# Kernel optimization log

Hardware: AMD Instinct MI355X
Metric: run time of the kernel (lower is better)

## Reference

```python
import jax, jax.numpy as jnp
import numpy as np

N_NODES = 50000
N_EDGES = 800000
D_FEAT = 128
HIDDEN = 128
BERT_DIM = 768
BATCH = 4096
MAX_ENT = 20
COMB = BERT_DIM + HIDDEN  # 896


def setup_inputs() -> dict:
    key = jax.random.key(0)
    ks = jax.random.split(key, 12)
    article_bert_embeddings = jax.random.normal(ks[0], (BATCH, BERT_DIM), dtype=jnp.float32)
    x = jax.random.normal(ks[1], (N_NODES, D_FEAT), dtype=jnp.float32)
    edge_index = jax.random.randint(ks[2], (2, N_EDGES), 0, N_NODES, dtype=jnp.int64)
    entity_map = jax.random.randint(ks[3], (BATCH, MAX_ENT), 0, N_NODES, dtype=jnp.int64)
    pad = jax.random.uniform(ks[4], (BATCH, MAX_ENT)) < 0.3
    entity_map = jnp.where(pad, jnp.int64(-1), entity_map)
    s = 1.0 / np.sqrt(D_FEAT)
    W1 = jax.random.normal(ks[5], (D_FEAT, HIDDEN), dtype=jnp.float32) * s
    b1 = jnp.zeros((HIDDEN,), dtype=jnp.float32)
    W2 = jax.random.normal(ks[6], (HIDDEN, HIDDEN), dtype=jnp.float32) * (1.0 / np.sqrt(HIDDEN))
    b2 = jnp.zeros((HIDDEN,), dtype=jnp.float32)
    fc1_w = jax.random.normal(ks[7], (COMB, COMB // 2), dtype=jnp.float32) * (1.0 / np.sqrt(COMB))
    fc1_b = jnp.zeros((COMB // 2,), dtype=jnp.float32)
    fc2_w = jax.random.normal(ks[8], (COMB // 2, 1), dtype=jnp.float32) * (1.0 / np.sqrt(COMB // 2))
    fc2_b = jnp.zeros((1,), dtype=jnp.float32)
    return dict(article_bert_embeddings=article_bert_embeddings, x=x,
                edge_index=edge_index, entity_map=entity_map,
                W1=W1, b1=b1, W2=W2, b2=b2,
                fc1_w=fc1_w, fc1_b=fc1_b, fc2_w=fc2_w, fc2_b=fc2_b)


def _gcn_norm(edge_index, n_nodes):
    # add self loops (PyG GCNConv default) and compute symmetric normalization
    loops = jnp.arange(n_nodes, dtype=edge_index.dtype)
    src = jnp.concatenate([edge_index[0], loops])
    dst = jnp.concatenate([edge_index[1], loops])
    deg = jax.ops.segment_sum(jnp.ones_like(dst, dtype=jnp.float32), dst, num_segments=n_nodes)
    dinv = jnp.where(deg > 0, jax.lax.rsqrt(deg), 0.0)
    norm = dinv[src] * dinv[dst]  # [E+N]
    return src, dst, norm


def _gcn_conv(h, W, b, src, dst, norm, n_nodes):
    h = h @ W                                   # [N, H] transform first (cheaper)
    msg = h[src] * norm[:, None]                # [E+N, H] gather
    out = jax.ops.segment_sum(msg, dst, num_segments=n_nodes)
    return out + b


def reference(article_bert_embeddings, x, edge_index, entity_map,
              W1, b1, W2, b2, fc1_w, fc1_b, fc2_w, fc2_b):
    n = x.shape[0]
    src, dst, norm = _gcn_norm(edge_index, n)
    # GNN (dropout in eval mode = identity)
    h = jax.nn.relu(_gcn_conv(x, W1, b1, src, dst, norm, n))
    h = jax.nn.relu(_gcn_conv(h, W2, b2, src, dst, norm, n))
    # ragged mean over entity lists (-1 = padding), fully vectorized
    mask = entity_map >= 0                           # [B, M]
    safe_ids = jnp.where(mask, entity_map, 0)
    gathered = h[safe_ids] * mask[..., None]         # [B, M, H]
    cnt = jnp.maximum(mask.sum(axis=1, keepdims=True).astype(h.dtype), 1.0)
    batch_gnn = gathered.sum(axis=1) / cnt           # [B, H]; rows w/ no entities stay 0
    combined = jnp.concatenate([article_bert_embeddings, batch_gnn], axis=1)
    z = jax.nn.relu(combined @ fc1_w + fc1_b)
    logits = z @ fc2_w + fc2_b
    return jax.nn.sigmoid(logits)
```

## Files before the change

### kernel.cpp

```cpp
#include <hip/hip_runtime.h>
#include <math.h>

typedef __bf16 bf16_t;
typedef __bf16 bfrag8 __attribute__((ext_vector_type(8)));
typedef float  facc4  __attribute__((ext_vector_type(4)));
typedef float  f32x2  __attribute__((ext_vector_type(2)));

#define NBUCK 512
#define BCAP  4096

__device__ inline unsigned short f2b(float x) {
    unsigned int u = __float_as_uint(x);
    unsigned int r = (u + 0x7fffu + ((u >> 16) & 1u)) >> 16;
    return (unsigned short)r;
}
__device__ inline unsigned int pack2(float lo, float hi) {
    return (unsigned int)f2b(lo) | ((unsigned int)f2b(hi) << 16);
}
__device__ inline float blo(unsigned int q) { return __uint_as_float(q << 16); }
__device__ inline float bhi(unsigned int q) { return __uint_as_float(q & 0xffff0000u); }

#if __has_builtin(__builtin_amdgcn_cvt_pk_f32_fp8) && __has_builtin(__builtin_amdgcn_cvt_pk_fp8_f32)
#define HW_FP8 1
#endif

__device__ inline f32x2 fp8pair_dec(unsigned short v) {
#ifdef HW_FP8
    return __builtin_amdgcn_cvt_pk_f32_fp8((int)(unsigned int)v, false);
#else
    f32x2 r;
    unsigned char b0 = (unsigned char)(v & 0xff), b1 = (unsigned char)(v >> 8);
    {
        int e = (b0 >> 3) & 0xf, m = b0 & 7;
        float mag = e ? ldexpf(8.f + m, e - 10) : ldexpf((float)m, -9);
        r.x = (b0 & 0x80) ? -mag : mag;
    }
    {
        int e = (b1 >> 3) & 0xf, m = b1 & 7;
        float mag = e ? ldexpf(8.f + m, e - 10) : ldexpf((float)m, -9);
        r.y = (b1 & 0x80) ? -mag : mag;
    }
    return r;
#endif
}
__device__ inline unsigned char fp8_enc(float x) {
#ifdef HW_FP8
    return (unsigned char)(__builtin_amdgcn_cvt_pk_fp8_f32(x, x, 0, false) & 0xff);
#else
    unsigned char s = (x < 0.f) ? 0x80 : 0;
    float ax = fabsf(x);
    if (!(ax > 0.f)) return s;
    if (ax >= 448.f) return s | 0x7e;
    if (ax < 0.015625f) {
        int q = (int)rintf(ax * 512.f);
        return s | (unsigned char)q;
    }
    int e; float m = frexpf(ax, &e);
    int q = (int)rintf(m * 16.f);
    int E = e - 1;
    if (q == 16) { q = 8; ++E; }
    if (E > 8) return s | 0x7e;
    return s | (unsigned char)(((E + 7) << 3) | (q - 8));
#endif
}

__device__ inline int bucket_of(int d, int N) {
    return (int)(((long long)d * NBUCK) / N);
}

__global__ __launch_bounds__(256) void k_prepbin(const int* __restrict__ src,
                                                 const int* __restrict__ dst,
                                                 int* __restrict__ bcnt,
                                                 unsigned int* __restrict__ ebuf,
                                                 int E, int N,
                                                 const float* __restrict__ bert,
                                                 unsigned int* __restrict__ bertb, int n8,
                                                 const float* __restrict__ W1,
                                                 unsigned short* __restrict__ w1t,
                                                 const float* __restrict__ W2,
                                                 unsigned short* __restrict__ w2t,
                                                 const float* __restrict__ Wf,
                                                 unsigned short* __restrict__ fwt) {
    __shared__ __align__(16) unsigned char smem[23552];
    int bb = blockIdx.x, tid = threadIdx.x;
    int nbin = (E + 4095) / 4096;
    if (bb < nbin) {
        unsigned int* sorted = (unsigned int*)smem;
        int* hist   = (int*)(smem + 16384);
        int* lstart = (int*)(smem + 18432);
        int* gbase  = (int*)(smem + 20480);
        int* sm     = (int*)(smem + 22528);
        int base = bb * 4096;
        int cnt = min(4096, E - base);
        hist[tid] = 0; hist[tid + 256] = 0;
        __syncthreads();
        unsigned int mye[16]; int myb[16];
#pragma unroll
        for (int i = 0; i < 16; ++i) {
            int idx = i * 256 + tid;
            myb[i] = -1;
            if (idx < cnt) {
                int e = base + idx;
                int s = src[e], d = dst[e];
                mye[i] = ((unsigned int)s << 16) | (unsigned int)d;
                int b = bucket_of(d, N);
                myb[i] = b;
                atomicAdd(&hist[b], 1);
            }
        }
        __syncthreads();
        int p0 = hist[2 * tid], p1 = hist[2 * tid + 1];
        sm[tid] = p0 + p1;
        __syncthreads();
        for (int off = 1; off < 256; off <<= 1) {
            int x = (tid >= off) ? sm[tid - off] : 0;
            __syncthreads();
            sm[tid] += x;
            __syncthreads();
        }
        int excl = sm[tid] - (p0 + p1);
        lstart[2 * tid] = excl;
        lstart[2 * tid + 1] = excl + p0;
        __syncthreads();
        hist[tid] = lstart[tid]; hist[tid + 256] = lstart[tid + 256];
        __syncthreads();
#pragma unroll
        for (int i = 0; i < 16; ++i) {
            if (myb[i] >= 0) {
                int pos = atomicAdd(&hist[myb[i]], 1);
                sorted[pos] = mye[i];
            }
        }
        __syncthreads();
        for (int b = tid; b < NBUCK; b += 256) {
            int c = hist[b] - lstart[b];
            gbase[b] = (c > 0) ? atomicAdd(&bcnt[b], c) : 0;
        }
        __syncthreads();
        for (int idx = tid; idx < cnt; idx += 256) {
            unsigned int v = sorted[idx];
            int b = bucket_of((int)(v & 0xffffu), N);
            ebuf[(size_t)b * BCAP + gbase[b] + (idx - lstart[b])] = v;
        }
        return;
    }
    bb -= nbin;
    int ncvt = (n8 + 255) / 256;
    if (bb < ncvt) {
        int i = bb * 256 + tid;
        if (i >= n8) return;
        const float4* p = (const float4*)bert + (size_t)i * 2;
        float4 a = p[0], b = p[1];
        uint4 o;
        o.x = pack2(a.x, a.y);
        o.y = pack2(a.z, a.w);
        o.z = pack2(b.x, b.y);
        o.w = pack2(b.z, b.w);
        ((uint4*)bertb)[i] = o;
        return;
    }
    bb -= ncvt;
    if (bb < 128) {
        int i = bb * 256 + tid;
        const float* W = (i < 16384) ? W1 : W2;
        unsigned short* Wt = (i < 16384) ? w1t : w2t;
        int idx = i & 16383;
        int n = idx >> 7, k = idx & 127;
        Wt[idx] = f2b(W[k * 128 + n]);
        return;
    }
    bb -= 128;
    {
        float* tile = (float*)smem;
        int n0 = (bb % 7) * 64, k0 = (bb / 7) * 64;
#pragma unroll
        for (int i = 0; i < 16; ++i) {
            int idx = i * 256 + tid;
            int r = idx >> 6, c = idx & 63;
            tile[r * 65 + c] = Wf[(size_t)(k0 + r) * 448 + n0 + c];
        }
        __syncthreads();
#pragma unroll
        for (int i = 0; i < 16; ++i) {
            int idx = i * 256 + tid;
            int c = idx >> 6, r = idx & 63;
            fwt[(size_t)(n0 + c) * 896 + k0 + r] = f2b(tile[r * 65 + c]);
        }
    }
}

__global__ __launch_bounds__(256) void k_build2(const unsigned int* __restrict__ ebuf,
                                                const int* __restrict__ bcnt,
                                                int* __restrict__ offs,
                                                float* __restrict__ dinv,
                                                unsigned short* __restrict__ csr,
                                                int N, int E) {
    __shared__ unsigned short seg[BCAP];
    __shared__ int cnt_l[128];
    __shared__ int scan_l[128];
    __shared__ int curs[128];
    __shared__ int smr[256];
    int b = blockIdx.x, tid = threadIdx.x;
    int part = 0;
    for (int j = tid; j < b; j += 256) part += bcnt[j];
    smr[tid] = part;
    __syncthreads();
    for (int off = 128; off > 0; off >>= 1) {
        if (tid < off) smr[tid] += smr[tid + off];
        __syncthreads();
    }
    int base = smr[0];
    int lo = (int)(((long long)b * N + NBUCK - 1) / NBUCK);
    int cnt = bcnt[b];
    int nrange = (int)(((long long)(b + 1) * N + NBUCK - 1) / NBUCK) - lo;
    if (b == 0 && tid == 0) offs[N] = E;
    if (tid < 128) cnt_l[tid] = 0;
    __syncthreads();
    for (int i = tid; i < cnt; i += 256) {
        unsigned int v = ebuf[(size_t)b * BCAP + i];
        atomicAdd(&cnt_l[(int)(v & 0xffffu) - lo], 1);
    }
    __syncthreads();
    if (tid < 128) scan_l[tid] = cnt_l[tid];
    __syncthreads();
    for (int off = 1; off < 128; off <<= 1) {
        int x = 0;
        if (tid < 128 && tid >= off) x = scan_l[tid - off];
        __syncthreads();
        if (tid < 128) scan_l[tid] += x;
        __syncthreads();
    }
    if (tid < 128) {
        int excl = scan_l[tid] - cnt_l[tid];
        curs[tid] = excl;
        if (tid < nrange) {
            offs[lo + tid] = base + excl;
            dinv[lo + tid] = rsqrtf((float)(cnt_l[tid] + 1));
        }
    }
    __syncthreads();
    for (int i = tid; i < cnt; i += 256) {
        unsigned int v = ebuf[(size_t)b * BCAP + i];
        int d = (int)(v & 0xffffu) - lo;
        int p = atomicAdd(&curs[d], 1);
        seg[p] = (unsigned short)(v >> 16);
    }
    __syncthreads();
    for (int i = tid; i < cnt; i += 256) csr[base + i] = seg[i];
}

__global__ __launch_bounds__(256) void k_gemm_f32a(const float* __restrict__ A,
                                                   const bf16_t* __restrict__ Bt,
                                                   const float* __restrict__ rs,
                                                   unsigned char* __restrict__ out8, int M) {
    __shared__ bf16_t As[64 * 136];
    __shared__ bf16_t Bs[128 * 136];
    int t = threadIdx.x;
    int wave = t >> 6, lane = t & 63, quad = lane >> 4, l16 = lane & 15;
    int r0 = blockIdx.x * 64;
#pragma unroll
    for (int i = 0; i < 4; ++i) {
        int chunk = t + i * 256;
        int row = chunk >> 4, c8 = (chunk & 15) << 3;
        int gr = r0 + row;
        float4 a0 = make_float4(0.f, 0.f, 0.f, 0.f), a1 = a0;
        if (gr < M) {
            a0 = *(const float4*)&A[(size_t)gr * 128 + c8];
            a1 = *(const float4*)&A[(size_t)gr * 128 + c8 + 4];
        }
        *(uint4*)&As[row * 136 + c8] =
            make_uint4(pack2(a0.x, a0.y), pack2(a0.z, a0.w),
                       pack2(a1.x, a1.y), pack2(a1.z, a1.w));
    }
#pragma unroll
    for (int i = 0; i < 8; ++i) {
        int chunk = t + i * 256;
        int row = chunk >> 4, c8 = (chunk & 15) << 3;
        *(uint4*)&Bs[row * 136 + c8] = *(const uint4*)&Bt[row * 128 + c8];
    }
    __syncthreads();

    facc4 acc[8];
#pragma unroll
    for (int nt = 0; nt < 8; ++nt) acc[nt] = (facc4){0.f, 0.f, 0.f, 0.f};
    int arow = (wave << 4) + l16;
#pragma unroll
    for (int ks = 0; ks < 4; ++ks) {
        int kk = ks * 32 + quad * 8;
        bfrag8 af = *(const bfrag8*)&As[arow * 136 + kk];
#pragma unroll
        for (int nt = 0; nt < 8; ++nt) {
            bfrag8 bf = *(const bfrag8*)&Bs[(nt * 16 + l16) * 136 + kk];
            acc[nt] = __builtin_amdgcn_mfma_f32_16x16x32_bf16(af, bf, acc[nt], 0, 0, 0);
        }
    }
    __syncthreads();
    unsigned char* f8t = (unsigned char*)As;
    int wrow0 = (wave << 4) + quad * 4;
#pragma unroll
    for (int r = 0; r < 4; ++r) {
        int row = wrow0 + r;
        float sc = rs[min(r0 + row, M - 1)];
#pragma unroll
        for (int nt = 0; nt < 8; ++nt)
            f8t[row * 128 + nt * 16 + l16] = fp8_enc(acc[nt][r] * sc);
    }
    __syncthreads();
#pragma unroll
    for (int i = 0; i < 2; ++i) {
        int idx = t + i * 256;
        int row = idx >> 3, cc = (idx & 7) << 4;
        int gr = r0 + row;
        if (gr < M) *(uint4*)&out8[(size_t)gr * 128 + cc] = *(const uint4*)&f8t[row * 128 + cc];
    }
}

__global__ __launch_bounds__(256) void k_gemm_nn128(const bf16_t* __restrict__ A,
                                                    const bf16_t* __restrict__ Bt,
                                                    const float* __restrict__ rs,
                                                    unsigned char* __restrict__ out8, int M) {
    __shared__ bf16_t As[64 * 136];
    __shared__ bf16_t Bs[128 * 136];
    int t = threadIdx.x;
    int wave = t >> 6, lane = t & 63, quad = lane >> 4, l16 = lane & 15;
    int r0 = blockIdx.x * 64;
#pragma unroll
    for (int i = 0; i < 4; ++i) {
        int chunk = t + i * 256;
        int row = chunk >> 4, c8 = (chunk & 15) << 3;
        int gr = r0 + row;
        uint4 v = make_uint4(0u, 0u, 0u, 0u);
        if (gr < M) v = *(const uint4*)&A[(size_t)gr * 128 + c8];
        *(uint4*)&As[row * 136 + c8] = v;
    }
#pragma unroll
    for (int i = 0; i < 8; ++i) {
        int chunk = t + i * 256;
        int row = chunk >> 4, c8 = (chunk & 15) << 3;
        *(uint4*)&Bs[row * 136 + c8] = *(const uint4*)&Bt[row * 128 + c8];
    }
    __syncthreads();

    facc4 acc[8];
#pragma unroll
    for (int nt = 0; nt < 8; ++nt) acc[nt] = (facc4){0.f, 0.f, 0.f, 0.f};
    int arow = (wave << 4) + l16;
#pragma unroll
    for (int ks = 0; ks < 4; ++ks) {
        int kk = ks * 32 + quad * 8;
        bfrag8 af = *(const bfrag8*)&As[arow * 136 + kk];
#pragma unroll
        for (int nt = 0; nt < 8; ++nt) {
            bfrag8 bf = *(const bfrag8*)&Bs[(nt * 16 + l16) * 136 + kk];
            acc[nt] = __builtin_amdgcn_mfma_f32_16x16x32_bf16(af, bf, acc[nt], 0, 0, 0);
        }
    }
    __syncthreads();
    unsigned char* f8t = (unsigned char*)As;
    int wrow0 = (wave << 4) + quad * 4;
#pragma unroll
    for (int r = 0; r < 4; ++r) {
        int row = wrow0 + r;
        float sc = rs[min(r0 + row, M - 1)];
#pragma unroll
        for (int nt = 0; nt < 8; ++nt)
            f8t[row * 128 + nt * 16 + l16] = fp8_enc(acc[nt][r] * sc);
    }
    __syncthreads();
#pragma unroll
    for (int i = 0; i < 2; ++i) {
        int idx = t + i * 256;
        int row = idx >> 3, cc = (idx & 7) << 4;
        int gr = r0 + row;
        if (gr < M) *(uint4*)&out8[(size_t)gr * 128 + cc] = *(const uint4*)&f8t[row * 128 + cc];
    }
}

__global__ __launch_bounds__(256) void k_agg_b(const unsigned short* __restrict__ hx8,
                                               const unsigned short* __restrict__ csr,
                                               const int* __restrict__ offs,
                                               const float* __restrict__ dinv,
                                               const float* __restrict__ bias,
                                               unsigned int* __restrict__ out, int N) {
    int node = blockIdx.x * 4 + (threadIdx.x >> 6);
    int lane = threadIdx.x & 63;
    if (node >= N) return;
    float di = dinv[node];
    f32x2 sf = fp8pair_dec(hx8[(size_t)node * 64 + lane]);
    float acc0 = sf.x, acc1 = sf.y;
    int s0 = offs[node], s1 = offs[node + 1];
    for (int base = s0; base < s1; base += 64) {
        int nloc = min(64, s1 - base);
        int en = 0;
        if (lane < nloc) en = (int)csr[base + lane];
        int j = 0;
        for (; j + 16 <= nloc; j += 16) {
            int sid[16]; unsigned short g[16];
#pragma unroll
            for (int u = 0; u < 16; ++u) sid[u] = __shfl(en, j + u, 64);
#pragma unroll
            for (int u = 0; u < 16; ++u) g[u] = hx8[(size_t)sid[u] * 64 + lane];
#pragma unroll
            for (int u = 0; u < 16; ++u) { f32x2 d = fp8pair_dec(g[u]); acc0 += d.x; acc1 += d.y; }
        }
        for (; j + 4 <= nloc; j += 4) {
            int sid[4]; unsigned short g[4];
#pragma unroll
            for (int u = 0; u < 4; ++u) sid[u] = __shfl(en, j + u, 64);
#pragma unroll
            for (int u = 0; u < 4; ++u) g[u] = hx8[(size_t)sid[u] * 64 + lane];
#pragma unroll
            for (int u = 0; u < 4; ++u) { f32x2 d = fp8pair_dec(g[u]); acc0 += d.x; acc1 += d.y; }
        }
        for (; j < nloc; ++j) {
            int srcn = __shfl(en, j, 64);
            f32x2 d = fp8pair_dec(hx8[(size_t)srcn * 64 + lane]);
            acc0 += d.x; acc1 += d.y;
        }
    }
    float2 bb = *(const float2*)&bias[lane * 2];
    float v0 = fmaxf(acc0 * di + bb.x, 0.f);
    float v1 = fmaxf(acc1 * di + bb.y, 0.f);
    out[(size_t)node * 64 + lane] = pack2(v0, v1);
}

__global__ __launch_bounds__(256) void k_pool_b(const unsigned int* __restrict__ h,
                                                const int* __restrict__ ent,
                                                unsigned int* __restrict__ out) {
    int r = blockIdx.x * 4 + (threadIdx.x >> 6);
    int lane = threadIdx.x & 63;
    float a0 = 0.f, a1 = 0.f;
    int cnt = 0;
#pragma unroll
    for (int m = 0; m < 20; ++m) {
        int id = ent[r * 20 + m];
        if (id >= 0) {
            unsigned int q = h[(size_t)id * 64 + lane];
            a0 += blo(q); a1 += bhi(q); cnt++;
        }
    }
    float inv = 1.f / (float)max(cnt, 1);
    out[(size_t)r * 64 + lane] = pack2(a0 * inv, a1 * inv);
}

__global__ __launch_bounds__(256) void k_mlp1_mfma(const bf16_t* __restrict__ bertb,
                                                   const bf16_t* __restrict__ gnnb,
                                                   const bf16_t* __restrict__ fwt,
                                                   const float* __restrict__ fb,
                                                   const float* __restrict__ w2,
                                                   float* __restrict__ logacc,
                                                   int* __restrict__ donecnt,
                                                   const float* __restrict__ b2,
                                                   float* __restrict__ outp, int B) {
    __shared__ bf16_t As[64 * 136];
    __shared__ bf16_t Bs[64 * 136];
    __shared__ int lastflag;
    int t = threadIdx.x;
    int wave = t >> 6, lane = t & 63, quad = lane >> 4, l16 = lane & 15;
    int r0 = blockIdx.x * 64, c0 = blockIdx.y * 64;
    facc4 acc[4];
#pragma unroll
    for (int nt = 0; nt < 4; ++nt) acc[nt] = (facc4){0.f, 0.f, 0.f, 0.f};

    for (int ks = 0; ks < 7; ++ks) {
#pragma unroll
        for (int i = 0; i < 4; ++i) {
            int chunk = t + i * 256;
            int row = chunk >> 4, c8 = (chunk & 15) << 3;
            int gr = r0 + row;
            const bf16_t* srcp = (ks < 6) ? &bertb[(size_t)gr * 768 + ks * 128 + c8]
                                          : &gnnb[(size_t)gr * 128 + c8];
            *(uint4*)&As[row * 136 + c8] = *(const uint4*)srcp;
        }
#pragma unroll
        for (int i = 0; i < 4; ++i) {
            int chunk = t + i * 256;
            int row = chunk >> 4, c8 = (chunk & 15) << 3;
            *(uint4*)&Bs[row * 136 + c8] =
                *(const uint4*)&fwt[(size_t)(c0 + row) * 896 + ks * 128 + c8];
        }
        __syncthreads();
        int arow = (wave << 4) + l16;
#pragma unroll
        for (int sub = 0; sub < 4; ++sub) {
            int kk = sub * 32 + quad * 8;
            bfrag8 af = *(const bfrag8*)&As[arow * 136 + kk];
#pragma unroll
            for (int nt = 0; nt < 4; ++nt) {
                bfrag8 bf = *(const bfrag8*)&Bs[(nt * 16 + l16) * 136 + kk];
                acc[nt] = __builtin_amdgcn_mfma_f32_16x16x32_bf16(af, bf, acc[nt], 0, 0, 0);
            }
        }
        __syncthreads();
    }
    int rbase = r0 + (wave << 4) + quad * 4;
    float part[4] = {0.f, 0.f, 0.f, 0.f};
#pragma unroll
    for (int nt = 0; nt < 4; ++nt) {
        int col = c0 + nt * 16 + l16;
        float bb = fb[col];
        float ww = w2[col];
#pragma unroll
        for (int r = 0; r < 4; ++r)
            part[r] += fmaxf(acc[nt][r] + bb, 0.f) * ww;
    }
#pragma unroll
    for (int m = 8; m >= 1; m >>= 1) {
#pragma unroll
        for (int r = 0; r < 4; ++r) part[r] += __shfl_xor(part[r], m, 64);
    }
    if (l16 == 0) {
#pragma unroll
        for (int r = 0; r < 4; ++r) atomicAdd(&logacc[rbase + r], part[r]);
    }
    __threadfence();
    __syncthreads();
    if (t == 0) {
        int done = atomicAdd(donecnt, 1);
        lastflag = (done == (int)(gridDim.x * gridDim.y) - 1);
    }
    __syncthreads();
    if (lastflag) {
        __threadfence();
        float bias2 = b2[0];
        for (int i = t; i < B; i += 256) {
            float v = atomicAdd(&logacc[i], 0.0f);
            outp[i] = 1.f / (1.f + expf(-(v + bias2)));
        }
    }
}

extern "C" void kernel_launch(void* const* d_in, const int* in_sizes, int n_in,
                              void* d_out, int out_size, void* d_ws, size_t ws_size,
                              hipStream_t stream) {
    const float* bert = (const float*)d_in[0];
    const float* x    = (const float*)d_in[1];
    const int*   ei   = (const int*)d_in[2];
    const int*   ent  = (const int*)d_in[3];
    const float* W1   = (const float*)d_in[4];
    const float* b1   = (const float*)d_in[5];
    const float* W2   = (const float*)d_in[6];
    const float* b2   = (const float*)d_in[7];
    const float* fc1w = (const float*)d_in[8];
    const float* fc1b = (const float*)d_in[9];
    const float* fc2w = (const float*)d_in[10];
    const float* fc2b = (const float*)d_in[11];
    float* out = (float*)d_out;

    const int N = in_sizes[1] / 128;
    const int E = in_sizes[2] / 2;
    const int B = in_sizes[0] / 768;

    const int* srcv = ei;
    const int* dstv = ei + E;

    char* wsp = (char*)d_ws;
    size_t off = 0;
    auto alloc = [&](size_t bytes) -> void* {
        void* p = wsp + off;
        off += (bytes + 255) & ~(size_t)255;
        return p;
    };
    int*   bcnt   = (int*)alloc(NBUCK * 4);
    float* logacc = (float*)alloc((size_t)B * 4);
    int*   donecnt= (int*)alloc(4);
    float* dinv   = (float*)alloc((size_t)N * 4);
    int*   offs   = (int*)alloc((size_t)(N + 1) * 4);
    unsigned int*   ebuf  = (unsigned int*)alloc((size_t)NBUCK * BCAP * 4);
    unsigned short* csr16 = (unsigned short*)alloc((size_t)E * 2);
    bf16_t* bertb = (bf16_t*)alloc((size_t)B * 768 * 2);
    bf16_t* w1t   = (bf16_t*)alloc(128 * 128 * 2);
    bf16_t* w2t   = (bf16_t*)alloc(128 * 128 * 2);
    bf16_t* fwt   = (bf16_t*)alloc((size_t)896 * 448 * 2);
    unsigned char* g8buf = (unsigned char*)alloc((size_t)N * 128);
    bf16_t* hbuf  = (bf16_t*)alloc((size_t)N * 128 * 2);
    bf16_t* gnnb  = (bf16_t*)alloc((size_t)B * 128 * 2);
    (void)ws_size; (void)n_in; (void)out_size;

    hipMemsetAsync(bcnt, 0, 2048 + 16384 + 256, stream);

    int nb8 = B * 768 / 8;
    int nbin = (E + 4095) / 4096;
    int nprep = nbin + (nb8 + 255) / 256 + 128 + 98;
    k_prepbin<<<nprep, 256, 0, stream>>>(srcv, dstv, bcnt, ebuf, E, N,
                                         bert, (unsigned int*)bertb, nb8,
                                         W1, (unsigned short*)w1t, W2, (unsigned short*)w2t,
                                         fc1w, (unsigned short*)fwt);
    k_build2<<<NBUCK, 256, 0, stream>>>(ebuf, bcnt, offs, dinv, csr16, N, E);

    int gb = (N + 63) / 64;
    k_gemm_f32a<<<gb, 256, 0, stream>>>(x, w1t, dinv, g8buf, N);
    k_agg_b<<<(N + 3) / 4, 256, 0, stream>>>((const unsigned short*)g8buf, csr16, offs, dinv, b1,
                                             (unsigned int*)hbuf, N);
    k_gemm_nn128<<<gb, 256, 0, stream>>>(hbuf, w2t, dinv, g8buf, N);
    k_agg_b<<<(N + 3) / 4, 256, 0, stream>>>((const unsigned short*)g8buf, csr16, offs, dinv, b2,
                                             (unsigned int*)hbuf, N);
    k_pool_b<<<B / 4, 256, 0, stream>>>((const unsigned int*)hbuf, ent, (unsigned int*)gnnb);
    k_mlp1_mfma<<<dim3(B / 64, 7), 256, 0, stream>>>(bertb, gnnb, fwt, fc1b, fc2w,
                                                     logacc, donecnt, fc2b, out, B);
}
```

Baseline: 243.8 us.

## Prefetch next K-slice into registers and halve MLP row tile in fc1 kernel

The fc1 MFMA kernel now uses 32-row tiles with 128 threads, which doubles the grid from 64x7 to 128x7 blocks so more CUs are busy. It also software-pipelines the K loop: the global loads for the next 128-wide K slice go into registers while MFMAs run on the current slice in LDS. The aim is to hide global-memory latency and improve occupancy. In exchange each block reloads the weight tile (B) for only half as many rows, and register use rises from the prefetch buffers.

```diff
diff --git a/kernel.cpp b/kernel.cpp
--- a/kernel.cpp
+++ b/kernel.cpp
@@ -443,7 +443,7 @@
     out[(size_t)r * 64 + lane] = pack2(a0 * inv, a1 * inv);
 }
 
-__global__ __launch_bounds__(256) void k_mlp1_mfma(const bf16_t* __restrict__ bertb,
+__global__ __launch_bounds__(128) void k_mlp1_mfma(const bf16_t* __restrict__ bertb,
                                                    const bf16_t* __restrict__ gnnb,
                                                    const bf16_t* __restrict__ fwt,
                                                    const float* __restrict__ fb,
@@ -452,34 +452,53 @@
                                                    int* __restrict__ donecnt,
                                                    const float* __restrict__ b2,
                                                    float* __restrict__ outp, int B) {
-    __shared__ bf16_t As[64 * 136];
+    __shared__ bf16_t As[32 * 136];
     __shared__ bf16_t Bs[64 * 136];
     __shared__ int lastflag;
     int t = threadIdx.x;
     int wave = t >> 6, lane = t & 63, quad = lane >> 4, l16 = lane & 15;
-    int r0 = blockIdx.x * 64, c0 = blockIdx.y * 64;
+    int r0 = blockIdx.x * 32, c0 = blockIdx.y * 64;
     facc4 acc[4];
 #pragma unroll
     for (int nt = 0; nt < 4; ++nt) acc[nt] = (facc4){0.f, 0.f, 0.f, 0.f};
 
+    uint4 pa[4], pb[8];
+#define LOAD_A(ks) do { \
+    _Pragma("unroll") \
+    for (int i = 0; i < 4; ++i) { \
+        int chunk = t + i * 128; \
+        int row = chunk >> 4, c8 = (chunk & 15) << 3; \
+        int gr = r0 + row; \
+        const bf16_t* srcp = ((ks) < 6) ? &bertb[(size_t)gr * 768 + (ks) * 128 + c8] \
+                                        : &gnnb[(size_t)gr * 128 + c8]; \
+        pa[i] = *(const uint4*)srcp; \
+    } } while (0)
+#define LOAD_B(ks) do { \
+    _Pragma("unroll") \
+    for (int i = 0; i < 8; ++i) { \
+        int chunk = t + i * 128; \
+        int row = chunk >> 4, c8 = (chunk & 15) << 3; \
+        pb[i] = *(const uint4*)&fwt[(size_t)(c0 + row) * 896 + (ks) * 128 + c8]; \
+    } } while (0)
+#define STORE_AB() do { \
+    _Pragma("unroll") \
+    for (int i = 0; i < 4; ++i) { \
+        int chunk = t + i * 128; \
+        int row = chunk >> 4, c8 = (chunk & 15) << 3; \
+        *(uint4*)&As[row * 136 + c8] = pa[i]; \
+    } \
+    _Pragma("unroll") \
+    for (int i = 0; i < 8; ++i) { \
+        int chunk = t + i * 128; \
+        int row = chunk >> 4, c8 = (chunk & 15) << 3; \
+        *(uint4*)&Bs[row * 136 + c8] = pb[i]; \
+    } } while (0)
+
+    LOAD_A(0); LOAD_B(0);
+    STORE_AB();
+    __syncthreads();
     for (int ks = 0; ks < 7; ++ks) {
-#pragma unroll
-        for (int i = 0; i < 4; ++i) {
-            int chunk = t + i * 256;
-            int row = chunk >> 4, c8 = (chunk & 15) << 3;
-            int gr = r0 + row;
-            const bf16_t* srcp = (ks < 6) ? &bertb[(size_t)gr * 768 + ks * 128 + c8]
-                                          : &gnnb[(size_t)gr * 128 + c8];
-            *(uint4*)&As[row * 136 + c8] = *(const uint4*)srcp;
-        }
-#pragma unroll
-        for (int i = 0; i < 4; ++i) {
-            int chunk = t + i * 256;
-            int row = chunk >> 4, c8 = (chunk & 15) << 3;
-            *(uint4*)&Bs[row * 136 + c8] =
-                *(const uint4*)&fwt[(size_t)(c0 + row) * 896 + ks * 128 + c8];
-        }
-        __syncthreads();
+        if (ks < 6) { LOAD_A(ks + 1); LOAD_B(ks + 1); }
         int arow = (wave << 4) + l16;
 #pragma unroll
         for (int sub = 0; sub < 4; ++sub) {
@@ -492,7 +511,11 @@
             }
         }
         __syncthreads();
-    }
+        if (ks < 6) { STORE_AB(); __syncthreads(); }
+    }
+#undef LOAD_A
+#undef LOAD_B
+#undef STORE_AB
     int rbase = r0 + (wave << 4) + quad * 4;
     float part[4] = {0.f, 0.f, 0.f, 0.f};
 #pragma unroll
@@ -523,7 +546,7 @@
     if (lastflag) {
         __threadfence();
         float bias2 = b2[0];
-        for (int i = t; i < B; i += 256) {
+        for (int i = t; i < B; i += 128) {
             float v = atomicAdd(&logacc[i], 0.0f);
             outp[i] = 1.f / (1.f + expf(-(v + bias2)));
         }
@@ -596,6 +619,6 @@
     k_agg_b<<<(N + 3) / 4, 256, 0, stream>>>((const unsigned short*)g8buf, csr16, offs, dinv, b2,
                                              (unsigned int*)hbuf, N);
     k_pool_b<<<B / 4, 256, 0, stream>>>((const unsigned int*)hbuf, ent, (unsigned int*)gnnb);
-    k_mlp1_mfma<<<dim3(B / 64, 7), 256, 0, stream>>>(bertb, gnnb, fwt, fc1b, fc2w,
+    k_mlp1_mfma<<<dim3(B / 32, 7), 128, 0, stream>>>(bertb, gnnb, fwt, fc1b, fc2w,
                                                      logacc, donecnt, fc2b, out, B);
 }
```

Measured after the change: 314.8 us. +29.1%, slower.

## Fuse bert fp32-to-bf16 conversion into MLP GEMM and split sigmoid kernel

Applied to the files above, without the earlier changes.

The separate prep-stage conversion of the bert embeddings to bf16 is removed. The MLP GEMM now reads fp32 bert directly and packs it to bf16 while loading the tile, which drops one write and one read of the bf16 copy. The GEMM tile is halved to 32 rows with 128 threads, doubling the block count. The last-block atomic completion counter and in-kernel sigmoid are replaced by a small separate sigmoid kernel, at the cost of an extra launch and the GEMM reading twice as many fp32 bytes for bert.

```diff
diff --git a/kernel.cpp b/kernel.cpp
--- a/kernel.cpp
+++ b/kernel.cpp
@@ -73,8 +73,6 @@
                                                  int* __restrict__ bcnt,
                                                  unsigned int* __restrict__ ebuf,
                                                  int E, int N,
-                                                 const float* __restrict__ bert,
-                                                 unsigned int* __restrict__ bertb, int n8,
                                                  const float* __restrict__ W1,
                                                  unsigned short* __restrict__ w1t,
                                                  const float* __restrict__ W2,
@@ -145,21 +143,6 @@
         return;
     }
     bb -= nbin;
-    int ncvt = (n8 + 255) / 256;
-    if (bb < ncvt) {
-        int i = bb * 256 + tid;
-        if (i >= n8) return;
-        const float4* p = (const float4*)bert + (size_t)i * 2;
-        float4 a = p[0], b = p[1];
-        uint4 o;
-        o.x = pack2(a.x, a.y);
-        o.y = pack2(a.z, a.w);
-        o.z = pack2(b.x, b.y);
-        o.w = pack2(b.z, b.w);
-        ((uint4*)bertb)[i] = o;
-        return;
-    }
-    bb -= ncvt;
     if (bb < 128) {
         int i = bb * 256 + tid;
         const float* W = (i < 16384) ? W1 : W2;
@@ -443,38 +426,42 @@
     out[(size_t)r * 64 + lane] = pack2(a0 * inv, a1 * inv);
 }
 
-__global__ __launch_bounds__(256) void k_mlp1_mfma(const bf16_t* __restrict__ bertb,
+__global__ __launch_bounds__(128) void k_mlp1_mfma(const float* __restrict__ bert,
                                                    const bf16_t* __restrict__ gnnb,
                                                    const bf16_t* __restrict__ fwt,
                                                    const float* __restrict__ fb,
                                                    const float* __restrict__ w2,
-                                                   float* __restrict__ logacc,
-                                                   int* __restrict__ donecnt,
-                                                   const float* __restrict__ b2,
-                                                   float* __restrict__ outp, int B) {
-    __shared__ bf16_t As[64 * 136];
+                                                   float* __restrict__ logacc) {
+    __shared__ bf16_t As[32 * 136];
     __shared__ bf16_t Bs[64 * 136];
-    __shared__ int lastflag;
     int t = threadIdx.x;
     int wave = t >> 6, lane = t & 63, quad = lane >> 4, l16 = lane & 15;
-    int r0 = blockIdx.x * 64, c0 = blockIdx.y * 64;
+    int r0 = blockIdx.x * 32, c0 = blockIdx.y * 64;
     facc4 acc[4];
 #pragma unroll
     for (int nt = 0; nt < 4; ++nt) acc[nt] = (facc4){0.f, 0.f, 0.f, 0.f};
 
     for (int ks = 0; ks < 7; ++ks) {
-#pragma unroll
-        for (int i = 0; i < 4; ++i) {
-            int chunk = t + i * 256;
-            int row = chunk >> 4, c8 = (chunk & 15) << 3;
-            int gr = r0 + row;
-            const bf16_t* srcp = (ks < 6) ? &bertb[(size_t)gr * 768 + ks * 128 + c8]
-                                          : &gnnb[(size_t)gr * 128 + c8];
-            *(uint4*)&As[row * 136 + c8] = *(const uint4*)srcp;
-        }
-#pragma unroll
-        for (int i = 0; i < 4; ++i) {
-            int chunk = t + i * 256;
+        if (ks < 6) {
+#pragma unroll
+            for (int i = 0; i < 8; ++i) {
+                int chunk = t + i * 128;
+                int row = chunk >> 5, c4 = (chunk & 31) << 2;
+                float4 a = *(const float4*)&bert[(size_t)(r0 + row) * 768 + ks * 128 + c4];
+                *(uint2*)&As[row * 136 + c4] = make_uint2(pack2(a.x, a.y), pack2(a.z, a.w));
+            }
+        } else {
+#pragma unroll
+            for (int i = 0; i < 4; ++i) {
+                int chunk = t + i * 128;
+                int row = chunk >> 4, c8 = (chunk & 15) << 3;
+                *(uint4*)&As[row * 136 + c8] =
+                    *(const uint4*)&gnnb[(size_t)(r0 + row) * 128 + c8];
+            }
+        }
+#pragma unroll
+        for (int i = 0; i < 8; ++i) {
+            int chunk = t + i * 128;
             int row = chunk >> 4, c8 = (chunk & 15) << 3;
             *(uint4*)&Bs[row * 136 + c8] =
                 *(const uint4*)&fwt[(size_t)(c0 + row) * 896 + ks * 128 + c8];
@@ -513,21 +500,12 @@
 #pragma unroll
         for (int r = 0; r < 4; ++r) atomicAdd(&logacc[rbase + r], part[r]);
     }
-    __threadfence();
-    __syncthreads();
-    if (t == 0) {
-        int done = atomicAdd(donecnt, 1);
-        lastflag = (done == (int)(gridDim.x * gridDim.y) - 1);
-    }
-    __syncthreads();
-    if (lastflag) {
-        __threadfence();
-        float bias2 = b2[0];
-        for (int i = t; i < B; i += 256) {
-            float v = atomicAdd(&logacc[i], 0.0f);
-            outp[i] = 1.f / (1.f + expf(-(v + bias2)));
-        }
-    }
+}
+
+__global__ void k_sig(const float* __restrict__ logacc, const float* __restrict__ b,
+                      float* __restrict__ out, int B) {
+    int i = blockIdx.x * 256 + threadIdx.x;
+    if (i < B) out[i] = 1.f / (1.f + expf(-(logacc[i] + b[0])));
 }
 
 extern "C" void kernel_launch(void* const* d_in, const int* in_sizes, int n_in,
@@ -563,12 +541,10 @@
     };
     int*   bcnt   = (int*)alloc(NBUCK * 4);
     float* logacc = (float*)alloc((size_t)B * 4);
-    int*   donecnt= (int*)alloc(4);
     float* dinv   = (float*)alloc((size_t)N * 4);
     int*   offs   = (int*)alloc((size_t)(N + 1) * 4);
     unsigned int*   ebuf  = (unsigned int*)alloc((size_t)NBUCK * BCAP * 4);
     unsigned short* csr16 = (unsigned short*)alloc((size_t)E * 2);
-    bf16_t* bertb = (bf16_t*)alloc((size_t)B * 768 * 2);
     bf16_t* w1t   = (bf16_t*)alloc(128 * 128 * 2);
     bf16_t* w2t   = (bf16_t*)alloc(128 * 128 * 2);
     bf16_t* fwt   = (bf16_t*)alloc((size_t)896 * 448 * 2);
@@ -577,13 +553,11 @@
     bf16_t* gnnb  = (bf16_t*)alloc((size_t)B * 128 * 2);
     (void)ws_size; (void)n_in; (void)out_size;
 
-    hipMemsetAsync(bcnt, 0, 2048 + 16384 + 256, stream);
-
-    int nb8 = B * 768 / 8;
+    hipMemsetAsync(bcnt, 0, 2048 + 16384, stream);
+
     int nbin = (E + 4095) / 4096;
-    int nprep = nbin + (nb8 + 255) / 256 + 128 + 98;
+    int nprep = nbin + 128 + 98;
     k_prepbin<<<nprep, 256, 0, stream>>>(srcv, dstv, bcnt, ebuf, E, N,
-                                         bert, (unsigned int*)bertb, nb8,
                                          W1, (unsigned short*)w1t, W2, (unsigned short*)w2t,
                                          fc1w, (unsigned short*)fwt);
     k_build2<<<NBUCK, 256, 0, stream>>>(ebuf, bcnt, offs, dinv, csr16, N, E);
@@ -596,6 +570,6 @@
     k_agg_b<<<(N + 3) / 4, 256, 0, stream>>>((const unsigned short*)g8buf, csr16, offs, dinv, b2,
                                              (unsigned int*)hbuf, N);
     k_pool_b<<<B / 4, 256, 0, stream>>>((const unsigned int*)hbuf, ent, (unsigned int*)gnnb);
-    k_mlp1_mfma<<<dim3(B / 64, 7), 256, 0, stream>>>(bertb, gnnb, fwt, fc1b, fc2w,
-                                                     logacc, donecnt, fc2b, out, B);
-}
+    k_mlp1_mfma<<<dim3(B / 32, 7), 128, 0, stream>>>(bert, gnnb, fwt, fc1b, fc2w, logacc);
+    k_sig<<<(B + 255) / 256, 256, 0, stream>>>(logacc, fc2b, out, B);
+}
```

Result: faster. 237.4 us (-2.6%).
